# Kernel optimization log

Measured on AMD Instinct MI355X. Metric: run time of the kernel, lower is better.

## Reference

```python
import jax, jax.numpy as jnp
import numpy as np

H = 8  # heads
EPS = 1e-5


def adaln(x, t, W, b):
    # AdaLayerNorm: emb = Linear(t); scale, shift = chunk(emb, 2, dim=-1)
    emb = t @ W + b                      # [B,1,2*D]
    scale, shift = jnp.split(emb, 2, axis=-1)
    mu = jnp.mean(x, axis=-1, keepdims=True)
    var = jnp.var(x, axis=-1, keepdims=True)
    xn = (x - mu) / jnp.sqrt(var + EPS)  # elementwise_affine=False
    return xn * (1.0 + scale) + shift


def attention(x, ctx, Wq, Wk, Wv, Wo, bo):
    B, N, D = x.shape
    d = D // H
    q = (x @ Wq).reshape(B, N, H, d).transpose(0, 2, 1, 3)          # [B,H,N,d]
    k = (ctx @ Wk).reshape(B, ctx.shape[1], H, d).transpose(0, 2, 1, 3)
    v = (ctx @ Wv).reshape(B, ctx.shape[1], H, d).transpose(0, 2, 1, 3)
    sim = jnp.einsum('bhid,bhjd->bhij', q, k) * (d ** -0.5)
    attn = jax.nn.softmax(sim, axis=-1)
    out = jnp.einsum('bhij,bhjd->bhid', attn, v)
    out = out.transpose(0, 2, 1, 3).reshape(B, N, D)
    return out @ Wo + bo


def geglu_ff(x, W1, b1, W2, b2):
    u, g = jnp.split(x @ W1 + b1, 2, axis=-1)
    return (u * jax.nn.gelu(g, approximate=False)) @ W2 + b2


def setup_inputs() -> dict:
    key = jax.random.key(0)
    ks = jax.random.split(key, 16)
    D = 512
    s = 0.02
    inp = {
        'x': jax.random.normal(ks[0], (2, 2048, D), jnp.float32),
        't': jax.random.normal(ks[1], (2, 1, D), jnp.float32),
        'cond': jax.random.normal(ks[2], (2, 1024, D), jnp.float32),
        'n1_w': jax.random.normal(ks[3], (D, 2 * D), jnp.float32) * s,
        'n1_b': jnp.zeros((2 * D,), jnp.float32),
        'n2_w': jax.random.normal(ks[4], (D, 2 * D), jnp.float32) * s,
        'n2_b': jnp.zeros((2 * D,), jnp.float32),
        'n4_w': jax.random.normal(ks[5], (D, 2 * D), jnp.float32) * s,
        'n4_b': jnp.zeros((2 * D,), jnp.float32),
        'a1_q': jax.random.normal(ks[6], (D, D), jnp.float32) * s,
        'a1_k': jax.random.normal(ks[7], (D, D), jnp.float32) * s,
        'a1_v': jax.random.normal(ks[8], (D, D), jnp.float32) * s,
        'a1_o': jax.random.normal(ks[9], (D, D), jnp.float32) * s,
        'a1_ob': jnp.zeros((D,), jnp.float32),
        'a2_q': jax.random.normal(ks[10], (D, D), jnp.float32) * s,
        'a2_k': jax.random.normal(ks[11], (D, D), jnp.float32) * s,
        'a2_v': jax.random.normal(ks[12], (D, D), jnp.float32) * s,
        'a2_o': jax.random.normal(ks[13], (D, D), jnp.float32) * s,
        'a2_ob': jnp.zeros((D,), jnp.float32),
        'ff_w1': jax.random.normal(ks[14], (D, 8 * D), jnp.float32) * s,
        'ff_b1': jnp.zeros((8 * D,), jnp.float32),
        'ff_w2': jax.random.normal(ks[15], (4 * D, D), jnp.float32) * s,
        'ff_b2': jnp.zeros((D,), jnp.float32),
    }
    return inp


def reference(x, t, cond, n1_w, n1_b, n2_w, n2_b, n4_w, n4_b,
              a1_q, a1_k, a1_v, a1_o, a1_ob,
              a2_q, a2_k, a2_v, a2_o, a2_ob,
              ff_w1, ff_b1, ff_w2, ff_b2):
    # BasicTransformerBlock, is_deform=False, withT=False, inference (dropout/droppath = identity, LayerScale = identity since init_values=0)
    h = adaln(x, t, n1_w, n1_b)
    x = attention(h, h, a1_q, a1_k, a1_v, a1_o, a1_ob) + x
    h = adaln(x, t, n2_w, n2_b)
    x = attention(h, cond, a2_q, a2_k, a2_v, a2_o, a2_ob) + x
    h = adaln(x, t, n4_w, n4_b)
    x = geglu_ff(h, ff_w1, ff_b1, ff_w2, ff_b2) + x
    return x
```

## Files before the change

### kernel.cpp

```cpp
#include <hip/hip_runtime.h>
#include <math.h>

#define D_MODEL 512
#define NHEADS  8
#define DHEAD   64

typedef __bf16  bf16x2 __attribute__((ext_vector_type(2)));
typedef __bf16  bf16x4 __attribute__((ext_vector_type(4)));
typedef __bf16  bf16x8 __attribute__((ext_vector_type(8)));
typedef float   f32x4  __attribute__((ext_vector_type(4)));
typedef float   f32x16 __attribute__((ext_vector_type(16)));

#define QSCALE 0.18033688f
#define DEFER_THR 11.5416f

__device__ __forceinline__ void gload16(const __bf16* g, __bf16* l) {
    __builtin_amdgcn_global_load_lds(
        (const __attribute__((address_space(1))) unsigned int*)g,
        (__attribute__((address_space(3))) unsigned int*)l, 16, 0, 0);
}

__device__ __forceinline__ void transpose_tile(
        const float* __restrict__ src, __bf16* __restrict__ dst,
        int K, int N, int k0, int n0) {
    __shared__ float t[64][65];
    int tid = threadIdx.x;
    int r = tid >> 6, c = tid & 63;
#pragma unroll
    for (int i = 0; i < 16; ++i)
        t[r + 4 * i][c] = src[(size_t)(k0 + r + 4 * i) * N + n0 + c];
    __syncthreads();
#pragma unroll
    for (int i = 0; i < 16; ++i)
        dst[(size_t)(n0 + r + 4 * i) * K + k0 + c] = (__bf16)t[c][r + 4 * i];
}

struct PrepArgs {
    const float *t, *n1w, *n1b, *n2w, *n2b, *n4w, *n4b;
    float* emb;
    const float* ws[8]; __bf16* wd[8];
    const float *ffw1, *ffw2;
    __bf16 *ff1t, *ff2t;
    const float* cond; __bf16* cbf;
    int B, condN;
};

__global__ __launch_bounds__(256) void prep_kernel(PrepArgs a) {
    int bb = blockIdx.x, tid = threadIdx.x;
    if (bb < 24) {
        int gI = bb * 256 + tid;
        int per = a.B * 2 * D_MODEL;
        if (gI >= 3 * per) return;
        int norm = gI / per;
        int rem  = gI - norm * per;
        int b = rem / (2 * D_MODEL);
        int c = rem % (2 * D_MODEL);
        const float* W  = (norm == 0) ? a.n1w : (norm == 1 ? a.n2w : a.n4w);
        const float* bb_= (norm == 0) ? a.n1b : (norm == 1 ? a.n2b : a.n4b);
        const float* trow = a.t + (size_t)b * D_MODEL;
        float acc = bb_[c];
        for (int k = 0; k < D_MODEL; ++k)
            acc = fmaf(trow[k], W[(size_t)k * (2 * D_MODEL) + c], acc);
        a.emb[gI] = acc;
    } else if (bb < 536) {
        int w = (bb - 24) >> 6, tI = (bb - 24) & 63;
        transpose_tile(a.ws[w], a.wd[w], 512, 512, (tI >> 3) << 6, (tI & 7) << 6);
    } else if (bb < 1048) {
        int tI = bb - 536;
        transpose_tile(a.ffw1, a.ff1t, 512, 4096, (tI & 7) << 6, (tI >> 3) << 6);
    } else if (bb < 1304) {
        int tI = bb - 1048;
        transpose_tile(a.ffw2, a.ff2t, 2048, 512, (tI >> 3) << 6, (tI & 7) << 6);
    } else {
        int i = ((bb - 1304) * 256 + tid) * 4;
        if (i >= a.condN) return;
        float4 v = *(const float4*)(a.cond + i);
        bf16x2 p0, p1;
        p0[0] = (__bf16)v.x; p0[1] = (__bf16)v.y;
        p1[0] = (__bf16)v.z; p1[1] = (__bf16)v.w;
        *(bf16x2*)(a.cbf + i)     = p0;
        *(bf16x2*)(a.cbf + i + 2) = p1;
    }
}

__global__ __launch_bounds__(256) void adaln_apply_kernel(
        const float* __restrict__ x, const float* __restrict__ emb_n,
        __bf16* __restrict__ h, int N) {
    int row = blockIdx.x;
    int b = row / N;
    const float* xr = x + (size_t)row * D_MODEL;
    int tid = threadIdx.x;
    float2 v = *(const float2*)(xr + 2 * tid);
    float s = v.x + v.y, sq = v.x * v.x + v.y * v.y;
#pragma unroll
    for (int off = 32; off; off >>= 1) {
        s  += __shfl_xor(s, off);
        sq += __shfl_xor(sq, off);
    }
    __shared__ float rs[4], rq[4];
    if ((tid & 63) == 0) { rs[tid >> 6] = s; rq[tid >> 6] = sq; }
    __syncthreads();
    float tot  = rs[0] + rs[1] + rs[2] + rs[3];
    float totq = rq[0] + rq[1] + rq[2] + rq[3];
    float mu  = tot * (1.0f / D_MODEL);
    float var = totq * (1.0f / D_MODEL) - mu * mu;
    float inv = rsqrtf(var + 1e-5f);
    const float* er = emb_n + (size_t)b * (2 * D_MODEL);
    float2 sc = *(const float2*)(er + 2 * tid);
    float2 sh = *(const float2*)(er + D_MODEL + 2 * tid);
    bf16x2 o;
    o[0] = (__bf16)((v.x - mu) * inv * (1.0f + sc.x) + sh.x);
    o[1] = (__bf16)((v.y - mu) * inv * (1.0f + sc.y) + sh.y);
    *(bf16x2*)(h + (size_t)row * D_MODEL + 2 * tid) = o;
}

template<int OUT, int WM>
__device__ __forceinline__ void gemm_body(
        const __bf16* __restrict__ A, const __bf16* __restrict__ Bt,
        const float* __restrict__ bias, const float* __restrict__ res,
        void* __restrict__ Cv, int M, int K, int N, int bx, int by,
        __bf16* As, __bf16* Bs) {
    constexpr int MI = WM / 16;
    int tid = threadIdx.x;
    int wave = tid >> 6, lane = tid & 63;
    int wr = wave >> 1, wc = wave & 1;
    int r = lane & 15, g = lane >> 4;
    int rx = r & 7;
    int m0 = by * (2 * WM), n0 = bx << 6;

    int lrow = lane >> 3;
    int lcol = ((lane & 7) ^ lrow) << 3;
    const __bf16* Ag = A  + (size_t)(m0 + (wave << 3) + lrow) * K + lcol;
    const __bf16* Bg = Bt + (size_t)(n0 + (wave << 3) + lrow) * K + lcol;
    __bf16* AsW = As + (size_t)(wave << 3) * 64;
    __bf16* BsW = Bs + (size_t)(wave << 3) * 64;

    f32x4 acc[MI][2];
#pragma unroll
    for (int mi = 0; mi < MI; ++mi)
#pragma unroll
        for (int ni = 0; ni < 2; ++ni) acc[mi][ni] = (f32x4){0.f, 0.f, 0.f, 0.f};

    for (int k0 = 0; k0 < K; k0 += 64) {
        if (k0) __syncthreads();
#pragma unroll
        for (int i = 0; i < MI; ++i)
            gload16(Ag + (size_t)(i * 32) * K + k0, AsW + i * 32 * 64);
#pragma unroll
        for (int j = 0; j < 2; ++j)
            gload16(Bg + (size_t)(j * 32) * K + k0, BsW + j * 32 * 64);
        __syncthreads();
#pragma unroll
        for (int kk = 0; kk < 2; ++kk) {
            int cs = ((((kk << 2) + g) ^ rx) << 3);
            bf16x8 af[MI], bf_[2];
#pragma unroll
            for (int mi = 0; mi < MI; ++mi)
                af[mi] = *(const bf16x8*)&As[(size_t)(wr * WM + (mi << 4) + r) * 64 + cs];
#pragma unroll
            for (int ni = 0; ni < 2; ++ni)
                bf_[ni] = *(const bf16x8*)&Bs[(size_t)((wc << 5) + (ni << 4) + r) * 64 + cs];
#pragma unroll
            for (int mi = 0; mi < MI; ++mi)
#pragma unroll
                for (int ni = 0; ni < 2; ++ni)
                    acc[mi][ni] = __builtin_amdgcn_mfma_f32_16x16x32_bf16(
                        af[mi], bf_[ni], acc[mi][ni], 0, 0, 0);
        }
    }

#pragma unroll
    for (int mi = 0; mi < MI; ++mi) {
#pragma unroll
        for (int ni = 0; ni < 2; ++ni) {
            int col = n0 + (wc << 5) + (ni << 4) + r;
            float scl = (OUT == 2 && col < 512) ? QSCALE : 1.0f;
#pragma unroll
            for (int rg = 0; rg < 4; ++rg) {
                int row = m0 + wr * WM + (mi << 4) + (g << 2) + rg;
                if (OUT == 1) {
                    float v = acc[mi][ni][rg] + bias[col] + res[(size_t)row * N + col];
                    ((float*)Cv)[(size_t)row * N + col] = v;
                } else {
                    ((__bf16*)Cv)[(size_t)row * N + col] = (__bf16)(acc[mi][ni][rg] * scl);
                }
            }
        }
    }
}

template<int OUT, int WM>
__global__ __launch_bounds__(256) void gemm_bf16_kernel(
        const __bf16* __restrict__ A, const __bf16* __restrict__ Bt,
        const float* __restrict__ bias, const float* __restrict__ res,
        void* __restrict__ Cv, int M, int K, int N) {
    __shared__ __attribute__((aligned(16))) __bf16 As[2 * WM * 64];
    __shared__ __attribute__((aligned(16))) __bf16 Bs[64 * 64];
    gemm_body<OUT, WM>(A, Bt, bias, res, Cv, M, K, N, blockIdx.x, blockIdx.y, As, Bs);
}

__global__ __launch_bounds__(256) void gemm_dual_kernel(
        const __bf16* A0, const __bf16* B0, __bf16* C0, int M0,
        const __bf16* A1, const __bf16* B1, __bf16* C1, int M1) {
    __shared__ __attribute__((aligned(16))) __bf16 As[64 * 64];
    __shared__ __attribute__((aligned(16))) __bf16 Bs[64 * 64];
    int nb0 = 8 * (M0 >> 6);
    if ((int)blockIdx.x < nb0) {
        gemm_body<2, 32>(A0, B0, nullptr, nullptr, C0, M0, 512, 512,
                         blockIdx.x & 7, blockIdx.x >> 3, As, Bs);
    } else {
        int id = blockIdx.x - nb0;
        gemm_body<0, 32>(A1, B1, nullptr, nullptr, C1, M1, 512, 1024,
                         id & 15, id >> 4, As, Bs);
    }
}

__global__ __launch_bounds__(256) void gemm_geglu_bf16_kernel(
        const __bf16* __restrict__ A, const __bf16* __restrict__ W1t,
        const float* __restrict__ b1, __bf16* __restrict__ gg, int M, int K) {
    const int NOUT = 4 * D_MODEL;
    __shared__ __attribute__((aligned(16))) __bf16 AsL[128 * 64];
    __shared__ __attribute__((aligned(16))) __bf16 BuL[64 * 64];
    __shared__ __attribute__((aligned(16))) __bf16 BgL[64 * 64];
    int tid = threadIdx.x;
    int wave = tid >> 6, lane = tid & 63;
    int wr = wave >> 1, wc = wave & 1;
    int r = lane & 15, g = lane >> 4;
    int rx = r & 7;
    int m0 = blockIdx.y << 7, n0 = blockIdx.x << 6;

    int lrow = lane >> 3;
    int lcol = ((lane & 7) ^ lrow) << 3;
    const __bf16* Ag = A   + (size_t)(m0 + (wave << 3) + lrow) * K + lcol;
    const __bf16* Ug = W1t + (size_t)(n0 + (wave << 3) + lrow) * K + lcol;
    const __bf16* Gg = W1t + (size_t)(NOUT + n0 + (wave << 3) + lrow) * K + lcol;
    __bf16* AsW = AsL + (size_t)(wave << 3) * 64;
    __bf16* BuW = BuL + (size_t)(wave << 3) * 64;
    __bf16* BgW = BgL + (size_t)(wave << 3) * 64;

    f32x4 accu[4][2], accg[4][2];
#pragma unroll
    for (int mi = 0; mi < 4; ++mi)
#pragma unroll
        for (int ni = 0; ni < 2; ++ni) {
            accu[mi][ni] = (f32x4){0.f, 0.f, 0.f, 0.f};
            accg[mi][ni] = (f32x4){0.f, 0.f, 0.f, 0.f};
        }

    for (int k0 = 0; k0 < K; k0 += 64) {
        if (k0) __syncthreads();
#pragma unroll
        for (int i = 0; i < 4; ++i)
            gload16(Ag + (size_t)(i * 32) * K + k0, AsW + i * 32 * 64);
#pragma unroll
        for (int j = 0; j < 2; ++j) {
            gload16(Ug + (size_t)(j * 32) * K + k0, BuW + j * 32 * 64);
            gload16(Gg + (size_t)(j * 32) * K + k0, BgW + j * 32 * 64);
        }
        __syncthreads();
#pragma unroll
        for (int kk = 0; kk < 2; ++kk) {
            int cs = ((((kk << 2) + g) ^ rx) << 3);
            bf16x8 af[4], bu[2], bg[2];
#pragma unroll
            for (int mi = 0; mi < 4; ++mi)
                af[mi] = *(const bf16x8*)&AsL[(size_t)((wr << 6) + (mi << 4) + r) * 64 + cs];
#pragma unroll
            for (int ni = 0; ni < 2; ++ni) {
                bu[ni] = *(const bf16x8*)&BuL[(size_t)((wc << 5) + (ni << 4) + r) * 64 + cs];
                bg[ni] = *(const bf16x8*)&BgL[(size_t)((wc << 5) + (ni << 4) + r) * 64 + cs];
            }
#pragma unroll
            for (int mi = 0; mi < 4; ++mi)
#pragma unroll
                for (int ni = 0; ni < 2; ++ni) {
                    accu[mi][ni] = __builtin_amdgcn_mfma_f32_16x16x32_bf16(
                        af[mi], bu[ni], accu[mi][ni], 0, 0, 0);
                    accg[mi][ni] = __builtin_amdgcn_mfma_f32_16x16x32_bf16(
                        af[mi], bg[ni], accg[mi][ni], 0, 0, 0);
                }
        }
    }

#pragma unroll
    for (int mi = 0; mi < 4; ++mi) {
#pragma unroll
        for (int ni = 0; ni < 2; ++ni) {
            int col = n0 + (wc << 5) + (ni << 4) + r;
            float bu_ = b1[col], bg_ = b1[NOUT + col];
#pragma unroll
            for (int rg = 0; rg < 4; ++rg) {
                int row = m0 + (wr << 6) + (mi << 4) + (g << 2) + rg;
                float u  = accu[mi][ni][rg] + bu_;
                float gv = accg[mi][ni][rg] + bg_;
                float ge = 0.5f * gv * (1.0f + erff(gv * 0.70710678118654752f));
                gg[(size_t)row * NOUT + col] = (__bf16)(u * ge);
            }
        }
    }
}

__global__ __launch_bounds__(256) void attn_mfma_kernel(
        const __bf16* __restrict__ q, const __bf16* __restrict__ k,
        const __bf16* __restrict__ v, __bf16* __restrict__ o,
        int Nq, int Nk, int sq, int skv) {
    __shared__ __attribute__((aligned(16))) __bf16 Ks[2][4096];
    __shared__ __attribute__((aligned(16))) __bf16 Vt[2][4096];
    __shared__ __attribute__((aligned(16))) __bf16 Pl[4][2048];

    int tid = threadIdx.x;
    int w = tid >> 6, lane = tid & 63;
    int c = lane & 31;
    int hg = lane >> 5;
    int cx = c & 7;

    int nwg = gridDim.x;
    int cpx = nwg >> 3;
    int bid = (int)blockIdx.x;
    int lb  = (bid & 7) * cpx + (bid >> 3);

    int nqb = Nq >> 7;
    int qb = lb % nqb;
    int hh = (lb / nqb) % NHEADS;
    int b  = lb / (nqb * NHEADS);

    const __bf16* qp = q + ((size_t)(b * Nq + (qb << 7) + (w << 5) + c)) * sq
                         + hh * DHEAD + (hg << 3);
    bf16x8 qf[4];
#pragma unroll
    for (int ks = 0; ks < 4; ++ks) qf[ks] = *(const bf16x8*)(qp + ks * 16);

    int krow = tid >> 2, kp_ = tid & 3;
    int va = tid & 31, vbb = tid >> 5;
    size_t kvbase = (size_t)b * Nk * skv + (size_t)hh * DHEAD;
    const __bf16* kp = k + kvbase + (size_t)krow * skv + (kp_ << 4);
    const __bf16* vp = v + kvbase + (size_t)(2 * va) * skv + (vbb << 3);
    int kwo0 = krow * 64 + ((((kp_ << 1) | 0) ^ (krow & 7)) << 3);
    int kwo1 = krow * 64 + ((((kp_ << 1) | 1) ^ (krow & 7)) << 3);
    int vwb  = vbb * 512 + ((va & 3) << 1);

    f32x16 oacc[2];
#pragma unroll
    for (int db = 0; db < 2; ++db)
#pragma unroll
        for (int rg = 0; rg < 16; ++rg) oacc[db][rg] = 0.f;
    float m = -1e30f, l = 0.f;
    f32x16 saccA[2], saccB[2];
    bf16x8 kr0, kr1, vr0, vr1;
    bf16x8 vf[2][4], pb[4];

    auto LOADREG = [&](int t) {
        const __bf16* kp2 = kp + (size_t)t * 64 * skv;
        const __bf16* vp2 = vp + (size_t)t * 64 * skv;
        kr0 = *(const bf16x8*)kp2; kr1 = *(const bf16x8*)(kp2 + 8);
        vr0 = *(const bf16x8*)vp2; vr1 = *(const bf16x8*)(vp2 + skv);
    };
    auto STAGEW = [&](int buf) {
        *(bf16x8*)&Ks[buf][kwo0] = kr0;
        *(bf16x8*)&Ks[buf][kwo1] = kr1;
#pragma unroll
        for (int j = 0; j < 8; ++j) {
            bf16x2 pr; pr[0] = vr0[j]; pr[1] = vr1[j];
            *(bf16x2*)&Vt[buf][vwb + j * 64 + (((va >> 2) ^ j) << 3)] = pr;
        }
    };
    auto QKT = [&](f32x16 (&sacc)[2], int buf) {
#pragma unroll
        for (int kb = 0; kb < 2; ++kb)
#pragma unroll
            for (int rg = 0; rg < 16; ++rg) sacc[kb][rg] = 0.f;
        __builtin_amdgcn_s_setprio(1);
#pragma unroll
        for (int kb = 0; kb < 2; ++kb) {
#pragma unroll
            for (int ks = 0; ks < 4; ++ks) {
                int row = (kb << 5) + c;
                bf16x8 kf = *(const bf16x8*)&Ks[buf][row * 64
                                + ((((ks << 1) + hg) ^ cx) << 3)];
                sacc[kb] = __builtin_amdgcn_mfma_f32_32x32x16_bf16(
                    kf, qf[ks], sacc[kb], 0, 0, 0);
            }
        }
        __builtin_amdgcn_s_setprio(0);
    };
    auto SMAX = [&](f32x16 (&sacc)[2]) {
        float mx = sacc[0][0];
#pragma unroll
        for (int kb = 0; kb < 2; ++kb)
#pragma unroll
            for (int rg = 0; rg < 16; ++rg) mx = fmaxf(mx, sacc[kb][rg]);
        mx = fmaxf(mx, __shfl_xor(mx, 32));
        if (!__all(mx <= m + DEFER_THR)) {
            float mn = fmaxf(m, mx);
            float al = exp2f(m - mn);
            m = mn; l *= al;
#pragma unroll
            for (int db = 0; db < 2; ++db)
#pragma unroll
                for (int rg = 0; rg < 16; ++rg) oacc[db][rg] *= al;
        }
        float sum = 0.f;
#pragma unroll
        for (int kb = 0; kb < 2; ++kb) {
#pragma unroll
            for (int rg4 = 0; rg4 < 4; ++rg4) {
                bf16x4 pk;
#pragma unroll
                for (int rr = 0; rr < 4; ++rr) {
                    float p = exp2f(sacc[kb][(rg4 << 2) + rr] - m);
                    sum += p;
                    pk[rr] = (__bf16)p;
                }
                int slot = (kb << 2) + rg4;
                *(bf16x4*)&Pl[w][c * 64 + ((slot ^ cx) << 3) + (hg << 2)] = pk;
            }
        }
        l += sum;
    };
    auto VFLOAD = [&](int buf) {
#pragma unroll
        for (int ks = 0; ks < 4; ++ks)
            pb[ks] = *(const bf16x8*)&Pl[w][c * 64 + ((((ks << 1) + hg) ^ cx) << 3)];
#pragma unroll
        for (int db = 0; db < 2; ++db)
#pragma unroll
            for (int ks = 0; ks < 4; ++ks) {
                int row = (db << 5) + c;
                vf[db][ks] = *(const bf16x8*)&Vt[buf][row * 64
                                + ((((ks << 1) + hg) ^ cx) << 3)];
            }
    };
    auto PVOP = [&]() {
        __builtin_amdgcn_s_setprio(1);
#pragma unroll
        for (int db = 0; db < 2; ++db)
#pragma unroll
            for (int ks = 0; ks < 4; ++ks)
                oacc[db] = __builtin_amdgcn_mfma_f32_32x32x16_bf16(
                    vf[db][ks], pb[ks], oacc[db], 0, 0, 0);
        __builtin_amdgcn_s_setprio(0);
    };

    int ntiles = Nk >> 6;
    LOADREG(0);
    STAGEW(0);
    LOADREG(1);
    __syncthreads();
    QKT(saccA, 0);

    for (int t = 0; t + 1 < ntiles; t += 2) {
        STAGEW(1);
        if (t + 2 < ntiles) LOADREG(t + 2);
        SMAX(saccA);
        VFLOAD(0);
        __syncthreads();
        QKT(saccB, 1);
        PVOP();
        if (t + 2 < ntiles) {
            STAGEW(0);
            if (t + 3 < ntiles) LOADREG(t + 3);
        }
        SMAX(saccB);
        VFLOAD(1);
        __syncthreads();
        if (t + 2 < ntiles) QKT(saccA, 0);
        PVOP();
    }

    l += __shfl_xor(l, 32);
    float inv = 1.0f / l;
    __bf16* ob = o + ((size_t)(b * Nq + (qb << 7) + (w << 5) + c)) * D_MODEL + hh * DHEAD;
#pragma unroll
    for (int db = 0; db < 2; ++db) {
#pragma unroll
        for (int rg4 = 0; rg4 < 4; ++rg4) {
            bf16x4 ov;
#pragma unroll
            for (int rr = 0; rr < 4; ++rr)
                ov[rr] = (__bf16)(oacc[db][(rg4 << 2) + rr] * inv);
            *(bf16x4*)&ob[(db << 5) + (rg4 << 3) + (hg << 2)] = ov;
        }
    }
}

extern "C" void kernel_launch(void* const* d_in, const int* in_sizes, int n_in,
                              void* d_out, int out_size, void* d_ws, size_t ws_size,
                              hipStream_t stream) {
    const float* x    = (const float*)d_in[0];
    const float* t    = (const float*)d_in[1];
    const float* cond = (const float*)d_in[2];
    const float* n1_w = (const float*)d_in[3];
    const float* n1_b = (const float*)d_in[4];
    const float* n2_w = (const float*)d_in[5];
    const float* n2_b = (const float*)d_in[6];
    const float* n4_w = (const float*)d_in[7];
    const float* n4_b = (const float*)d_in[8];
    const float* a1_q = (const float*)d_in[9];
    const float* a1_k = (const float*)d_in[10];
    const float* a1_v = (const float*)d_in[11];
    const float* a1_o = (const float*)d_in[12];
    const float* a1_ob= (const float*)d_in[13];
    const float* a2_q = (const float*)d_in[14];
    const float* a2_k = (const float*)d_in[15];
    const float* a2_v = (const float*)d_in[16];
    const float* a2_o = (const float*)d_in[17];
    const float* a2_ob= (const float*)d_in[18];
    const float* ff_w1= (const float*)d_in[19];
    const float* ff_b1= (const float*)d_in[20];
    const float* ff_w2= (const float*)d_in[21];
    const float* ff_b2= (const float*)d_in[22];
    float* out = (float*)d_out;

    const int B  = in_sizes[1] / D_MODEL;
    const int N  = in_sizes[0] / (B * D_MODEL);
    const int Nc = in_sizes[2] / (B * D_MODEL);
    const int R  = B * N;
    const int Rc = B * Nc;

    char* Wb = (char*)d_ws;
    float* emb   = (float*)Wb;
    __bf16* r1   = (__bf16*)(Wb + 32768);
    __bf16* qkv  = r1;
    __bf16* q2   = r1;
    __bf16* kv2  = r1 + (size_t)R * 512;
    __bf16* gg   = r1;
    __bf16* h_bf = (__bf16*)(Wb + 32768 + 16777216);
    __bf16* c_bf = (__bf16*)(Wb + 32768 + 16777216 + 4194304);
    __bf16* wts  = (__bf16*)(Wb + 32768 + 16777216 + 4194304 + 2097152);
    __bf16* a1_qt = wts;
    __bf16* a1_ot = wts + 3 * 262144;
    __bf16* a2_qt = wts + 4 * 262144;
    __bf16* a2_kt = wts + 5 * 262144;
    __bf16* a2_ot = wts + 7 * 262144;
    __bf16* ff1t  = wts + 8 * 262144;
    __bf16* ff2t  = ff1t + 2097152;

    dim3 blk(256);

    PrepArgs pa;
    pa.t = t; pa.n1w = n1_w; pa.n1b = n1_b; pa.n2w = n2_w; pa.n2b = n2_b;
    pa.n4w = n4_w; pa.n4b = n4_b; pa.emb = emb;
    pa.ws[0] = a1_q; pa.ws[1] = a1_k; pa.ws[2] = a1_v; pa.ws[3] = a1_o;
    pa.ws[4] = a2_q; pa.ws[5] = a2_k; pa.ws[6] = a2_v; pa.ws[7] = a2_o;
    pa.wd[0] = a1_qt; pa.wd[1] = wts + 262144; pa.wd[2] = wts + 2 * 262144; pa.wd[3] = a1_ot;
    pa.wd[4] = a2_qt; pa.wd[5] = a2_kt; pa.wd[6] = wts + 6 * 262144; pa.wd[7] = a2_ot;
    pa.ffw1 = ff_w1; pa.ffw2 = ff_w2; pa.ff1t = ff1t; pa.ff2t = ff2t;
    pa.cond = cond; pa.cbf = c_bf; pa.B = B; pa.condN = Rc * D_MODEL;
    prep_kernel<<<dim3(1304 + (Rc * D_MODEL) / 1024), blk, 0, stream>>>(pa);

    adaln_apply_kernel<<<dim3(R), blk, 0, stream>>>(x, emb, h_bf, N);
    gemm_bf16_kernel<2, 64><<<dim3(24, R / 128), blk, 0, stream>>>(
        h_bf, a1_qt, nullptr, nullptr, qkv, R, 512, 1536);
    attn_mfma_kernel<<<dim3(B * NHEADS * (N / 128)), dim3(256), 0, stream>>>(
        qkv, qkv + 512, qkv + 1024, h_bf, N, N, 1536, 1536);
    gemm_bf16_kernel<1, 32><<<dim3(8, R / 64), blk, 0, stream>>>(
        h_bf, a1_ot, a1_ob, x, out, R, 512, 512);

    adaln_apply_kernel<<<dim3(R), blk, 0, stream>>>(
        out, emb + (size_t)B * 2 * D_MODEL, h_bf, N);
    gemm_dual_kernel<<<dim3(8 * (R / 64) + 16 * (Rc / 64)), blk, 0, stream>>>(
        h_bf, a2_qt, q2, R, c_bf, a2_kt, kv2, Rc);
    attn_mfma_kernel<<<dim3(B * NHEADS * (N / 128)), dim3(256), 0, stream>>>(
        q2, kv2, kv2 + 512, h_bf, N, Nc, 512, 1024);
    gemm_bf16_kernel<1, 32><<<dim3(8, R / 64), blk, 0, stream>>>(
        h_bf, a2_ot, a2_ob, out, out, R, 512, 512);

    adaln_apply_kernel<<<dim3(R), blk, 0, stream>>>(
        out, emb + (size_t)2 * B * 2 * D_MODEL, h_bf, N);
    gemm_geglu_bf16_kernel<<<dim3(32, R / 128), blk, 0, stream>>>(
        h_bf, ff1t, ff_b1, gg, R, 512);
    gemm_bf16_kernel<1, 32><<<dim3(8, R / 64), blk, 0, stream>>>(
        gg, ff2t, ff_b2, out, out, R, 2048, 512);
}
```

Before: 230.0 us.

## Split attention KV across two blocks with 512-thread workgroups and merge kernel

Attention now uses 512-thread blocks covering 256 query rows, and the KV sequence is split in half across grid.y (split-K / flash-decoding style). Each split writes unnormalized partial outputs plus per-row max and sum to scratch, and a new merge kernel rescales and combines them. K and V staging is divided between the two halves of the threads, and the LDS swizzles are changed to reduce bank conflicts. The goal is more parallelism and better occupancy, at the cost of extra memory traffic, bf16 rounding of unnormalized partials, and one extra launch per attention.

```diff
diff --git a/kernel.cpp b/kernel.cpp
--- a/kernel.cpp
+++ b/kernel.cpp
@@ -300,44 +300,52 @@
     }
 }
 
-__global__ __launch_bounds__(256) void attn_mfma_kernel(
+__global__ __launch_bounds__(512) void attn_mfma_kernel(
         const __bf16* __restrict__ q, const __bf16* __restrict__ k,
-        const __bf16* __restrict__ v, __bf16* __restrict__ o,
+        const __bf16* __restrict__ v, __bf16* __restrict__ op0,
+        __bf16* __restrict__ op1, float* __restrict__ ml,
         int Nq, int Nk, int sq, int skv) {
     __shared__ __attribute__((aligned(16))) __bf16 Ks[2][4096];
     __shared__ __attribute__((aligned(16))) __bf16 Vt[2][4096];
-    __shared__ __attribute__((aligned(16))) __bf16 Pl[4][2048];
+    __shared__ __attribute__((aligned(16))) __bf16 Pl[8][2048];
 
     int tid = threadIdx.x;
     int w = tid >> 6, lane = tid & 63;
     int c = lane & 31;
     int hg = lane >> 5;
     int cx = c & 7;
+    int sxp = cx ^ (c >> 3);
 
     int nwg = gridDim.x;
     int cpx = nwg >> 3;
     int bid = (int)blockIdx.x;
     int lb  = (bid & 7) * cpx + (bid >> 3);
 
-    int nqb = Nq >> 7;
+    int split = blockIdx.y;
+    int kvlen = Nk >> 1;
+
+    int nqb = Nq >> 8;
     int qb = lb % nqb;
     int hh = (lb / nqb) % NHEADS;
     int b  = lb / (nqb * NHEADS);
 
-    const __bf16* qp = q + ((size_t)(b * Nq + (qb << 7) + (w << 5) + c)) * sq
+    const __bf16* qp = q + ((size_t)(b * Nq + (qb << 8) + (w << 5) + c)) * sq
                          + hh * DHEAD + (hg << 3);
     bf16x8 qf[4];
 #pragma unroll
     for (int ks = 0; ks < 4; ++ks) qf[ks] = *(const bf16x8*)(qp + ks * 16);
 
-    int krow = tid >> 2, kp_ = tid & 3;
-    int va = tid & 31, vbb = tid >> 5;
-    size_t kvbase = (size_t)b * Nk * skv + (size_t)hh * DHEAD;
+    bool isK = (tid >= 256);
+    int sidx = tid & 255;
+    int krow = sidx >> 2, kp_ = sidx & 3;
+    int va = sidx & 31, vbb = sidx >> 5;
+    size_t kvbase = (size_t)b * Nk * skv + (size_t)hh * DHEAD
+                  + (size_t)split * kvlen * skv;
     const __bf16* kp = k + kvbase + (size_t)krow * skv + (kp_ << 4);
     const __bf16* vp = v + kvbase + (size_t)(2 * va) * skv + (vbb << 3);
-    int kwo0 = krow * 64 + ((((kp_ << 1) | 0) ^ (krow & 7)) << 3);
-    int kwo1 = krow * 64 + ((((kp_ << 1) | 1) ^ (krow & 7)) << 3);
-    int vwb  = vbb * 512 + ((va & 3) << 1);
+    int ksx  = (krow & 7) ^ (krow >> 3);
+    int kwo0 = krow * 64 + ((((kp_ << 1) | 0) ^ ksx) << 3);
+    int kwo1 = krow * 64 + ((((kp_ << 1) | 1) ^ ksx) << 3);
 
     f32x16 oacc[2];
 #pragma unroll
@@ -346,22 +354,30 @@
         for (int rg = 0; rg < 16; ++rg) oacc[db][rg] = 0.f;
     float m = -1e30f, l = 0.f;
     f32x16 saccA[2], saccB[2];
-    bf16x8 kr0, kr1, vr0, vr1;
+    bf16x8 sr0, sr1;
     bf16x8 vf[2][4], pb[4];
 
     auto LOADREG = [&](int t) {
-        const __bf16* kp2 = kp + (size_t)t * 64 * skv;
-        const __bf16* vp2 = vp + (size_t)t * 64 * skv;
-        kr0 = *(const bf16x8*)kp2; kr1 = *(const bf16x8*)(kp2 + 8);
-        vr0 = *(const bf16x8*)vp2; vr1 = *(const bf16x8*)(vp2 + skv);
+        if (isK) {
+            const __bf16* kp2 = kp + (size_t)t * 64 * skv;
+            sr0 = *(const bf16x8*)kp2; sr1 = *(const bf16x8*)(kp2 + 8);
+        } else {
+            const __bf16* vp2 = vp + (size_t)t * 64 * skv;
+            sr0 = *(const bf16x8*)vp2; sr1 = *(const bf16x8*)(vp2 + skv);
+        }
     };
     auto STAGEW = [&](int buf) {
-        *(bf16x8*)&Ks[buf][kwo0] = kr0;
-        *(bf16x8*)&Ks[buf][kwo1] = kr1;
-#pragma unroll
-        for (int j = 0; j < 8; ++j) {
-            bf16x2 pr; pr[0] = vr0[j]; pr[1] = vr1[j];
-            *(bf16x2*)&Vt[buf][vwb + j * 64 + (((va >> 2) ^ j) << 3)] = pr;
+        if (isK) {
+            *(bf16x8*)&Ks[buf][kwo0] = sr0;
+            *(bf16x8*)&Ks[buf][kwo1] = sr1;
+        } else {
+#pragma unroll
+            for (int j = 0; j < 8; ++j) {
+                bf16x2 pr; pr[0] = sr0[j]; pr[1] = sr1[j];
+                *(bf16x2*)&Vt[buf][vbb * 512 + j * 64
+                                   + ((((va >> 2) ^ j ^ vbb) & 7) << 3)
+                                   + ((va & 3) << 1)] = pr;
+            }
         }
     };
     auto QKT = [&](f32x16 (&sacc)[2], int buf) {
@@ -372,11 +388,12 @@
         __builtin_amdgcn_s_setprio(1);
 #pragma unroll
         for (int kb = 0; kb < 2; ++kb) {
+            int row = (kb << 5) + c;
+            int sxk = cx ^ (((kb << 2) + (c >> 3)) & 7);
 #pragma unroll
             for (int ks = 0; ks < 4; ++ks) {
-                int row = (kb << 5) + c;
                 bf16x8 kf = *(const bf16x8*)&Ks[buf][row * 64
-                                + ((((ks << 1) + hg) ^ cx) << 3)];
+                                + ((((ks << 1) + hg) ^ sxk) << 3)];
                 sacc[kb] = __builtin_amdgcn_mfma_f32_32x32x16_bf16(
                     kf, qf[ks], sacc[kb], 0, 0, 0);
             }
@@ -412,7 +429,7 @@
                     pk[rr] = (__bf16)p;
                 }
                 int slot = (kb << 2) + rg4;
-                *(bf16x4*)&Pl[w][c * 64 + ((slot ^ cx) << 3) + (hg << 2)] = pk;
+                *(bf16x4*)&Pl[w][c * 64 + ((slot ^ sxp) << 3) + (hg << 2)] = pk;
             }
         }
         l += sum;
@@ -420,15 +437,16 @@
     auto VFLOAD = [&](int buf) {
 #pragma unroll
         for (int ks = 0; ks < 4; ++ks)
-            pb[ks] = *(const bf16x8*)&Pl[w][c * 64 + ((((ks << 1) + hg) ^ cx) << 3)];
-#pragma unroll
-        for (int db = 0; db < 2; ++db)
-#pragma unroll
-            for (int ks = 0; ks < 4; ++ks) {
-                int row = (db << 5) + c;
+            pb[ks] = *(const bf16x8*)&Pl[w][c * 64 + ((((ks << 1) + hg) ^ sxp) << 3)];
+#pragma unroll
+        for (int db = 0; db < 2; ++db) {
+            int row = (db << 5) + c;
+            int sxv = cx ^ (((db << 2) + (c >> 3)) & 7);
+#pragma unroll
+            for (int ks = 0; ks < 4; ++ks)
                 vf[db][ks] = *(const bf16x8*)&Vt[buf][row * 64
-                                + ((((ks << 1) + hg) ^ cx) << 3)];
-            }
+                                + ((((ks << 1) + hg) ^ sxv) << 3)];
+        }
     };
     auto PVOP = [&]() {
         __builtin_amdgcn_s_setprio(1);
@@ -441,7 +459,7 @@
         __builtin_amdgcn_s_setprio(0);
     };
 
-    int ntiles = Nk >> 6;
+    int ntiles = kvlen >> 6;
     LOADREG(0);
     STAGEW(0);
     LOADREG(1);
@@ -468,8 +486,9 @@
     }
 
     l += __shfl_xor(l, 32);
-    float inv = 1.0f / l;
-    __bf16* ob = o + ((size_t)(b * Nq + (qb << 7) + (w << 5) + c)) * D_MODEL + hh * DHEAD;
+    int rowq = (qb << 8) + (w << 5) + c;
+    __bf16* ob = (split ? op1 : op0)
+               + ((size_t)(b * Nq + rowq)) * D_MODEL + hh * DHEAD;
 #pragma unroll
     for (int db = 0; db < 2; ++db) {
 #pragma unroll
@@ -477,10 +496,38 @@
             bf16x4 ov;
 #pragma unroll
             for (int rr = 0; rr < 4; ++rr)
-                ov[rr] = (__bf16)(oacc[db][(rg4 << 2) + rr] * inv);
+                ov[rr] = (__bf16)oacc[db][(rg4 << 2) + rr];
             *(bf16x4*)&ob[(db << 5) + (rg4 << 3) + (hg << 2)] = ov;
         }
     }
+    if (hg == 0) {
+        size_t mi_ = ((((size_t)(b * NHEADS + hh) * Nq + rowq) << 1) + split) << 1;
+        ml[mi_]     = m;
+        ml[mi_ + 1] = l;
+    }
+}
+
+__global__ __launch_bounds__(256) void attn_merge_kernel(
+        const __bf16* __restrict__ p0, const __bf16* __restrict__ p1,
+        const float* __restrict__ ml, __bf16* __restrict__ out, int Nq) {
+    int i = blockIdx.x * 256 + threadIdx.x;
+    int oct = i & 63, rowg = i >> 6;
+    int b = rowg / Nq, row = rowg - b * Nq;
+    int h = oct >> 3;
+    size_t mb = (((size_t)(b * NHEADS + h) * Nq + row) << 2);
+    float m0 = ml[mb], l0 = ml[mb + 1], m1 = ml[mb + 2], l1 = ml[mb + 3];
+    float mm = fmaxf(m0, m1);
+    float a0 = exp2f(m0 - mm), a1 = exp2f(m1 - mm);
+    float inv = 1.0f / (a0 * l0 + a1 * l1);
+    a0 *= inv; a1 *= inv;
+    size_t off = (size_t)rowg * D_MODEL + oct * 8;
+    bf16x8 x0 = *(const bf16x8*)(p0 + off);
+    bf16x8 x1 = *(const bf16x8*)(p1 + off);
+    bf16x8 o;
+#pragma unroll
+    for (int j = 0; j < 8; ++j)
+        o[j] = (__bf16)(a0 * (float)x0[j] + a1 * (float)x1[j]);
+    *(bf16x8*)(out + off) = o;
 }
 
 extern "C" void kernel_launch(void* const* d_in, const int* in_sizes, int n_in,
@@ -524,6 +571,9 @@
     __bf16* q2   = r1;
     __bf16* kv2  = r1 + (size_t)R * 512;
     __bf16* gg   = r1;
+    __bf16* p0s  = r1 + (size_t)R * 1536;
+    __bf16* p0c  = r1 + (size_t)4 * 1048576;
+    __bf16* p1c  = r1 + (size_t)6 * 1048576;
     __bf16* h_bf = (__bf16*)(Wb + 32768 + 16777216);
     __bf16* c_bf = (__bf16*)(Wb + 32768 + 16777216 + 4194304);
     __bf16* wts  = (__bf16*)(Wb + 32768 + 16777216 + 4194304 + 2097152);
@@ -534,6 +584,7 @@
     __bf16* a2_ot = wts + 7 * 262144;
     __bf16* ff1t  = wts + 8 * 262144;
     __bf16* ff2t  = ff1t + 2097152;
+    float* mlbuf = (float*)(Wb + 32768 + 16777216 + 4194304 + 2097152 + 10485760);
 
     dim3 blk(256);
 
@@ -551,8 +602,10 @@
     adaln_apply_kernel<<<dim3(R), blk, 0, stream>>>(x, emb, h_bf, N);
     gemm_bf16_kernel<2, 64><<<dim3(24, R / 128), blk, 0, stream>>>(
         h_bf, a1_qt, nullptr, nullptr, qkv, R, 512, 1536);
-    attn_mfma_kernel<<<dim3(B * NHEADS * (N / 128)), dim3(256), 0, stream>>>(
-        qkv, qkv + 512, qkv + 1024, h_bf, N, N, 1536, 1536);
+    attn_mfma_kernel<<<dim3(B * NHEADS * (N / 256), 2), dim3(512), 0, stream>>>(
+        qkv, qkv + 512, qkv + 1024, p0s, h_bf, mlbuf, N, N, 1536, 1536);
+    attn_merge_kernel<<<dim3(R * 64 / 256), blk, 0, stream>>>(
+        p0s, h_bf, mlbuf, h_bf, N);
     gemm_bf16_kernel<1, 32><<<dim3(8, R / 64), blk, 0, stream>>>(
         h_bf, a1_ot, a1_ob, x, out, R, 512, 512);
 
@@ -560,8 +613,10 @@
         out, emb + (size_t)B * 2 * D_MODEL, h_bf, N);
     gemm_dual_kernel<<<dim3(8 * (R / 64) + 16 * (Rc / 64)), blk, 0, stream>>>(
         h_bf, a2_qt, q2, R, c_bf, a2_kt, kv2, Rc);
-    attn_mfma_kernel<<<dim3(B * NHEADS * (N / 128)), dim3(256), 0, stream>>>(
-        q2, kv2, kv2 + 512, h_bf, N, Nc, 512, 1024);
+    attn_mfma_kernel<<<dim3(B * NHEADS * (N / 256), 2), dim3(512), 0, stream>>>(
+        q2, kv2, kv2 + 512, p0c, p1c, mlbuf, N, Nc, 512, 1024);
+    attn_merge_kernel<<<dim3(R * 64 / 256), blk, 0, stream>>>(
+        p0c, p1c, mlbuf, h_bf, N);
     gemm_bf16_kernel<1, 32><<<dim3(8, R / 64), blk, 0, stream>>>(
         h_bf, a2_ot, a2_ob, out, out, R, 512, 512);
 
```

Measured after the change: 233.1 us. Within noise of the previous version (+1.4%).
